# Kernel tuning notes

Measured on AMD Instinct MI355X. Metric: run time of the kernel, lower is better.

The kernel has to match this reference:

```python
import jax, jax.numpy as jnp
import numpy as np

B, T, C, H = 4, 2048, 1024, 16
HD = C // H

def setup_inputs() -> dict:
    key = jax.random.key(0)
    ks = jax.random.split(key, 9)
    s = 1.0 / np.sqrt(C)
    return {
        'x':  jax.random.normal(ks[0], (B, T, C), jnp.float32),
        'Wq': jax.random.normal(ks[1], (C, C), jnp.float32) * s,
        'bq': jnp.zeros((C,), jnp.float32),
        'Wk': jax.random.normal(ks[2], (C, C), jnp.float32) * s,
        'bk': jnp.zeros((C,), jnp.float32),
        'Wv': jax.random.normal(ks[3], (C, C), jnp.float32) * s,
        'bv': jnp.zeros((C,), jnp.float32),
        'Wo': jax.random.normal(ks[4], (C, C), jnp.float32) * s,
        'bo': jnp.zeros((C,), jnp.float32),
    }

def reference(x, Wq, bq, Wk, bk, Wv, bv, Wo, bo):
    Bx, Tx, Cx = x.shape
    # projections (torch Linear: x @ W.T + b); split heads -> (B,H,T,HD)
    def heads(y):
        return y.reshape(Bx, Tx, H, HD).transpose(0, 2, 1, 3)
    q = heads(x @ Wq.T + bq)
    k = heads(x @ Wk.T + bk)
    v = heads(x @ Wv.T + bv)
    # NOTE: original scales by 1/sqrt(embedding_dim), not head_dim
    scale = 1.0 / jnp.sqrt(jnp.asarray(Cx, x.dtype))
    att = jnp.einsum('bhqd,bhkd->bhqk', q, k) * scale
    mask = jnp.tril(jnp.ones((Tx, Tx), dtype=bool))
    att = jnp.where(mask, att, jnp.asarray(-jnp.inf, att.dtype))
    att = jax.nn.softmax(att, axis=-1)
    y = jnp.einsum('bhqk,bhkd->bhqd', att, v)
    y = y.transpose(0, 2, 1, 3).reshape(Bx, Tx, Cx)
    return y @ Wo.T + bo
```

## Files before the change

### kernel.cpp

```cpp
#include <hip/hip_runtime.h>
#include <hip/hip_bf16.h>
#include <stdint.h>

#define NB 4
#define NT 2048
#define NC 1024
#define NH 16
#define NHD 64
#define NM (NB*NT)

typedef __attribute__((ext_vector_type(8))) __bf16 bf16x8;
typedef __attribute__((ext_vector_type(4))) float floatx4;
typedef __attribute__((ext_vector_type(8))) unsigned short ushortx8;

#define AS1(p) ((const __attribute__((address_space(1))) void*)(p))
#define AS3(p) ((__attribute__((address_space(3))) void*)(p))

__device__ __forceinline__ unsigned short f2bf(float f) {
    union { float f; unsigned int u; } v; v.f = f;
    unsigned int u = v.u;
    return (unsigned short)((u + 0x7FFFu + ((u >> 16) & 1u)) >> 16);
}
__device__ __forceinline__ unsigned int pk2(float lo, float hi) {
    union { float f; unsigned int u; } a, b; a.f = hi; b.f = lo;
    return __builtin_amdgcn_perm(a.u, b.u, 0x07060302u);
}


__global__ void cast_x_tiled(const float* __restrict__ in,
                             unsigned short* __restrict__ out, int ntiles) {
    const int wid  = (blockIdx.x * blockDim.x + threadIdx.x) >> 6;
    const int lane = threadIdx.x & 63;
    if (wid >= ntiles) return;
    const int R = wid >> 5, C = wid & 31;
    const float* src = in + ((size_t)(R*16 + (lane >> 2)))*1024 + C*32 + (lane & 3)*8;
    const floatx4 v0 = *(const floatx4*)src;
    const floatx4 v1 = *(const floatx4*)(src + 4);
    ushortx8 o;
    o[0] = f2bf(v0[0]); o[1] = f2bf(v0[1]); o[2] = f2bf(v0[2]); o[3] = f2bf(v0[3]);
    o[4] = f2bf(v1[0]); o[5] = f2bf(v1[1]); o[6] = f2bf(v1[2]); o[7] = f2bf(v1[3]);
    *(ushortx8*)&out[(size_t)wid*512 + (((lane & 3)*16 + (lane >> 2)))*8] = o;
}

__global__ void cast4_tiled(const float* __restrict__ w0, const float* __restrict__ w1,
                            const float* __restrict__ w2, const float* __restrict__ w3,
                            unsigned short* __restrict__ o0, unsigned short* __restrict__ o1,
                            unsigned short* __restrict__ o2, unsigned short* __restrict__ o3,
                            int ntiles) {
    const int wid  = (blockIdx.x * blockDim.x + threadIdx.x) >> 6;
    const int lane = threadIdx.x & 63;
    if (wid >= ntiles) return;
    const float* in; unsigned short* out;
    switch (blockIdx.y) {
        case 0: in = w0; out = o0; break;
        case 1: in = w1; out = o1; break;
        case 2: in = w2; out = o2; break;
        default: in = w3; out = o3; break;
    }
    const int R = wid >> 5, C = wid & 31;
    const float* src = in + ((size_t)(R*16 + (lane >> 2)))*1024 + C*32 + (lane & 3)*8;
    const floatx4 v0 = *(const floatx4*)src;
    const floatx4 v1 = *(const floatx4*)(src + 4);
    ushortx8 o;
    o[0] = f2bf(v0[0]); o[1] = f2bf(v0[1]); o[2] = f2bf(v0[2]); o[3] = f2bf(v0[3]);
    o[4] = f2bf(v1[0]); o[5] = f2bf(v1[1]); o[6] = f2bf(v1[2]); o[7] = f2bf(v1[3]);
    *(ushortx8*)&out[(size_t)wid*512 + (((lane & 3)*16 + (lane >> 2)))*8] = o;
}

#define TM 128
#define TN 128
#define BK 32

__device__ __forceinline__ void gemm_core(
    const unsigned short* __restrict__ A,
    const unsigned short* __restrict__ W,
    const float* __restrict__ bias,
    void* __restrict__ Out,
    unsigned short* As, unsigned short* Bs,
    int m_base, int n_base, int N_out, int K, int mode, float oscale)
{
    const int tid  = threadIdx.x;
    const int lane = tid & 63;
    const int wv   = tid >> 6;
    const int quad = lane >> 4;
    const int l16  = lane & 15;
    const int wm = (wv >> 1) * 64;
    const int wn = (wv & 1) * 64;

    floatx4 acc[4][4];
    #pragma unroll
    for (int i = 0; i < 4; ++i)
        #pragma unroll
        for (int j = 0; j < 4; ++j)
            acc[i][j] = (floatx4){0.f, 0.f, 0.f, 0.f};

    const int kTiles = K / BK;
    const int kct = K >> 5;

    const unsigned short* At = A + ((size_t)((m_base >> 4) + wv*2) * kct) * 512 + (size_t)lane*8;
    const unsigned short* Wt = W + ((size_t)((n_base >> 4) + wv*2) * kct) * 512 + (size_t)lane*8;
    const size_t rstride = (size_t)kct * 512;

    for (int kt = 0; kt < kTiles; ++kt) {
        __syncthreads();
        #pragma unroll
        for (int i = 0; i < 2; ++i) {
            __builtin_amdgcn_global_load_lds(
                AS1(At + (size_t)kt*512 + i*rstride),
                AS3(&As[(wv*2 + i)*512]), 16, 0, 0);
            __builtin_amdgcn_global_load_lds(
                AS1(Wt + (size_t)kt*512 + i*rstride),
                AS3(&Bs[(wv*2 + i)*512]), 16, 0, 0);
        }
        __syncthreads();

        bf16x8 af[4], bfr[4];
        #pragma unroll
        for (int mi = 0; mi < 4; ++mi)
            af[mi] = *(const bf16x8*)&As[((wv >> 1)*4 + mi)*512 + lane*8];
        #pragma unroll
        for (int ni = 0; ni < 4; ++ni)
            bfr[ni] = *(const bf16x8*)&Bs[((wv & 1)*4 + ni)*512 + lane*8];

        #pragma unroll
        for (int mi = 0; mi < 4; ++mi)
            #pragma unroll
            for (int ni = 0; ni < 4; ++ni)
                acc[mi][ni] = __builtin_amdgcn_mfma_f32_16x16x32_bf16(
                    af[mi], bfr[ni], acc[mi][ni], 0, 0, 0);
    }

    #pragma unroll
    for (int mi = 0; mi < 4; ++mi) {
        #pragma unroll
        for (int ni = 0; ni < 4; ++ni) {
            const int col = n_base + wn + ni*16 + l16;
            const float bv = bias[col & 1023];
            #pragma unroll
            for (int r = 0; r < 4; ++r) {
                const int row = m_base + wm + mi*16 + quad*4 + r;
                const float v = (acc[mi][ni][r] + bv) * oscale;
                if (mode == 0) {
                    ((float*)Out)[(size_t)row * N_out + col] = v;
                } else if (mode == 1) {
                    const int bb = row >> 11, t = row & (NT - 1);
                    const int h  = (col >> 6) & (NH - 1), d = col & 63;
                    const int bh = bb * NH + h;
                    const size_t idx =
                        ((size_t)((bh*128 + (t >> 4))*2 + (d >> 5)))*512
                        + (size_t)((((d >> 3) & 3)*16 + (t & 15))*8 + (d & 7));
                    ((unsigned short*)Out)[idx] = f2bf(v);
                } else {
                    const int bb = row >> 11, t = row & (NT - 1);
                    const int h  = (col >> 6) & (NH - 1), hd = col & 63;
                    const int bh = bb * NH + h;
                    const int tk = t & 31;
                    const int qv = (tk >> 2) & 3;
                    const int jv = (tk & 3) + ((tk >> 4) << 2);
                    const size_t idx =
                        ((size_t)((bh*64 + (t >> 5))*4 + (hd >> 4)))*512
                        + (size_t)((qv*16 + (hd & 15))*8 + jv);
                    ((unsigned short*)Out)[idx] = f2bf(v);
                }
            }
        }
    }
}

#define QSCALE (0.03125f * 1.44269504088896340736f)

__global__ __launch_bounds__(256) void gemm_qkv(
    const unsigned short* __restrict__ A,
    const unsigned short* __restrict__ Wq, const unsigned short* __restrict__ Wk,
    const unsigned short* __restrict__ Wv,
    const float* __restrict__ bq, const float* __restrict__ bk,
    const float* __restrict__ bv,
    unsigned short* __restrict__ Qo, unsigned short* __restrict__ Ko,
    unsigned short* __restrict__ Vo)
{
    __shared__ __align__(16) unsigned short As[TM*BK];
    __shared__ __align__(16) unsigned short Bs[TN*BK];
    const int wi = blockIdx.y >> 3;
    const int n_base = (blockIdx.y & 7) * TN;
    const unsigned short* W; const float* bias; void* Out; int mode; float osc;
    if (wi == 0)      { W = Wq; bias = bq; Out = Qo; mode = 1; osc = QSCALE; }
    else if (wi == 1) { W = Wk; bias = bk; Out = Ko; mode = 1; osc = 1.0f; }
    else              { W = Wv; bias = bv; Out = Vo; mode = 2; osc = 1.0f; }
    gemm_core(A, W, bias, Out, As, Bs, blockIdx.x * TM, n_base, NC, NC, mode, osc);
}

__global__ __launch_bounds__(256) void gemm_out(
    const unsigned short* __restrict__ A,
    const unsigned short* __restrict__ W,
    const float* __restrict__ bias,
    float* __restrict__ Out)
{
    __shared__ __align__(16) unsigned short As[TM*BK];
    __shared__ __align__(16) unsigned short Bs[TN*BK];
    gemm_core(A, W, bias, Out, As, Bs, blockIdx.x * TM, blockIdx.y * TN,
              NC, NC, 0, 1.0f);
}

__device__ __forceinline__ void attn_q32(
    const unsigned short* __restrict__ Qf,
    const unsigned short* __restrict__ Kf,
    const unsigned short* __restrict__ Vf,
    unsigned short* __restrict__ Y,
    int bh, int st, int lane)
{
    const int quad = lane >> 4, l16 = lane & 15;
    const int q0 = st * 32;
    const int b = bh >> 4, h = bh & (NH - 1);

    const size_t qbase = ((size_t)(bh*128 + st*2))*1024 + (size_t)lane*8;
    const bf16x8 qa0 = *(const bf16x8*)&Qf[qbase];
    const bf16x8 qa1 = *(const bf16x8*)&Qf[qbase + 512];
    const bf16x8 qb0 = *(const bf16x8*)&Qf[qbase + 1024];
    const bf16x8 qb1 = *(const bf16x8*)&Qf[qbase + 1536];

    const unsigned short* kp = Kf + (size_t)bh*131072 + (size_t)lane*8;
    const unsigned short* vp = Vf + (size_t)bh*131072 + (size_t)lane*8;

    floatx4 oa[4], ob[4];
    #pragma unroll
    for (int nt = 0; nt < 4; ++nt) {
        oa[nt] = (floatx4){0.f,0.f,0.f,0.f};
        ob[nt] = (floatx4){0.f,0.f,0.f,0.f};
    }
    float la = 0.f, lb = 0.f;

    const int Ffull = q0 >> 6;
    const int ntile = Ffull + 1;

    for (int f = 0; f < ntile; ++f) {
        const int j0 = f * 64;
        const bool diag = (f == Ffull);
        bf16x8 kf[4][2], vf[4][2];
        {
            const unsigned short* kt = kp + (size_t)(j0 >> 4) * 1024;
            #pragma unroll
            for (int ct = 0; ct < 4; ++ct) {
                kf[ct][0] = *(const bf16x8*)&kt[ct*1024];
                kf[ct][1] = *(const bf16x8*)&kt[ct*1024 + 512];
            }
            const unsigned short* vt = vp + (size_t)(j0 >> 5) * 2048;
            #pragma unroll
            for (int nt = 0; nt < 4; ++nt) {
                vf[nt][0] = *(const bf16x8*)&vt[nt*512];
                vf[nt][1] = *(const bf16x8*)&vt[2048 + nt*512];
            }
        }
        #pragma unroll
        for (int sub = 0; sub < 2; ++sub) {
            const bf16x8 qx0 = sub ? qb0 : qa0;
            const bf16x8 qx1 = sub ? qb1 : qa1;
            floatx4* ox = sub ? ob : oa;

            floatx4 s[4];
            #pragma unroll
            for (int ct = 0; ct < 4; ++ct) {
                s[ct] = (floatx4){0.f,0.f,0.f,0.f};
                s[ct] = __builtin_amdgcn_mfma_f32_16x16x32_bf16(kf[ct][0], qx0, s[ct], 0,0,0);
                s[ct] = __builtin_amdgcn_mfma_f32_16x16x32_bf16(kf[ct][1], qx1, s[ct], 0,0,0);
            }
            float p[4][4];
            float lsum = 0.f;
            if (!diag) {
                #pragma unroll
                for (int ct = 0; ct < 4; ++ct)
                    #pragma unroll
                    for (int r = 0; r < 4; ++r) {
                        p[ct][r] = __builtin_amdgcn_exp2f(s[ct][r]);
                        lsum += p[ct][r];
                    }
            } else {
                const int row = q0 + sub*16 + l16;
                #pragma unroll
                for (int ct = 0; ct < 4; ++ct)
                    #pragma unroll
                    for (int r = 0; r < 4; ++r) {
                        const int key = j0 + ct*16 + quad*4 + r;
                        p[ct][r] = (key <= row) ? __builtin_amdgcn_exp2f(s[ct][r]) : 0.f;
                        lsum += p[ct][r];
                    }
            }
            if (sub) lb += lsum; else la += lsum;

            union { bf16x8 v; unsigned int u[4]; } pf0, pf1;
            pf0.u[0] = pk2(p[0][0], p[0][1]); pf0.u[1] = pk2(p[0][2], p[0][3]);
            pf0.u[2] = pk2(p[1][0], p[1][1]); pf0.u[3] = pk2(p[1][2], p[1][3]);
            pf1.u[0] = pk2(p[2][0], p[2][1]); pf1.u[1] = pk2(p[2][2], p[2][3]);
            pf1.u[2] = pk2(p[3][0], p[3][1]); pf1.u[3] = pk2(p[3][2], p[3][3]);

            #pragma unroll
            for (int nt = 0; nt < 4; ++nt) {
                ox[nt] = __builtin_amdgcn_mfma_f32_16x16x32_bf16(vf[nt][0], pf0.v, ox[nt], 0,0,0);
                ox[nt] = __builtin_amdgcn_mfma_f32_16x16x32_bf16(vf[nt][1], pf1.v, ox[nt], 0,0,0);
            }
        }
    }

    la += __shfl_xor(la, 16); la += __shfl_xor(la, 32);
    lb += __shfl_xor(lb, 16); lb += __shfl_xor(lb, 32);
    const float ia = 1.0f / la, ib = 1.0f / lb;

    const size_t Rbase = (size_t)((b*NT + q0) >> 4);
    const int cg = (quad >> 1), co = (quad & 1)*4;
    #pragma unroll
    for (int nt = 0; nt < 4; ++nt) {
        const size_t base = ((Rbase*32 + h*2 + (nt >> 1))*512)
                          + (size_t)((((nt & 1)*2 + cg)*16 + l16)*8 + co);
        ushort4 wa, wb;
        wa.x = f2bf(oa[nt][0]*ia); wa.y = f2bf(oa[nt][1]*ia);
        wa.z = f2bf(oa[nt][2]*ia); wa.w = f2bf(oa[nt][3]*ia);
        wb.x = f2bf(ob[nt][0]*ib); wb.y = f2bf(ob[nt][1]*ib);
        wb.z = f2bf(ob[nt][2]*ib); wb.w = f2bf(ob[nt][3]*ib);
        *(ushort4*)&Y[base]         = wa;
        *(ushort4*)&Y[base + 16384] = wb;
    }
}

__global__ __launch_bounds__(256) void flash_attn(
    const unsigned short* __restrict__ Qf,
    const unsigned short* __restrict__ Kf,
    const unsigned short* __restrict__ Vf,
    unsigned short* __restrict__ Y)
{
    const int tid  = threadIdx.x;
    const int wave = tid >> 6;
    const int lane = tid & 63;
    const int bh = blockIdx.y;
    const int w = blockIdx.x * 4 + wave;
    attn_q32(Qf, Kf, Vf, Y, bh, w, lane);
    attn_q32(Qf, Kf, Vf, Y, bh, 63 - w, lane);
}

extern "C" void kernel_launch(void* const* d_in, const int* in_sizes, int n_in,
                              void* d_out, int out_size, void* d_ws, size_t ws_size,
                              hipStream_t stream) {
    const float* x  = (const float*)d_in[0];
    const float* Wq = (const float*)d_in[1];
    const float* bq = (const float*)d_in[2];
    const float* Wk = (const float*)d_in[3];
    const float* bk = (const float*)d_in[4];
    const float* Wv = (const float*)d_in[5];
    const float* bv = (const float*)d_in[6];
    const float* Wo = (const float*)d_in[7];
    const float* bo = (const float*)d_in[8];

    char* ws = (char*)d_ws;
    size_t off = 0;
    auto alloc = [&](size_t bytes) -> void* {
        void* p = ws + off;
        off += (bytes + 255) & ~(size_t)255;
        return p;
    };
    unsigned short* xb  = (unsigned short*)alloc((size_t)NM * NC * 2);
    unsigned short* Wqb = (unsigned short*)alloc((size_t)NC * NC * 2);
    unsigned short* Wkb = (unsigned short*)alloc((size_t)NC * NC * 2);
    unsigned short* Wvb = (unsigned short*)alloc((size_t)NC * NC * 2);
    unsigned short* Wob = (unsigned short*)alloc((size_t)NC * NC * 2);
    unsigned short* Qb  = (unsigned short*)alloc((size_t)NM * NC * 2);
    unsigned short* Kb  = (unsigned short*)alloc((size_t)NM * NC * 2);
    unsigned short* Vtb = (unsigned short*)alloc((size_t)NM * NC * 2);
    unsigned short* Yb  = (unsigned short*)alloc((size_t)NM * NC * 2);

    const int ntx = NM * NC / 512;
    const int ntw = NC * NC / 512;
    cast_x_tiled<<<(ntx*64 + 255)/256, 256, 0, stream>>>(x, xb, ntx);
    cast4_tiled<<<dim3((ntw*64 + 255)/256, 4), 256, 0, stream>>>(
        Wq, Wk, Wv, Wo, Wqb, Wkb, Wvb, Wob, ntw);

    gemm_qkv<<<dim3(NM / TM, 24), 256, 0, stream>>>(
        xb, Wqb, Wkb, Wvb, bq, bk, bv, Qb, Kb, Vtb);

    flash_attn<<<dim3(8, NB*NH), 256, 0, stream>>>(Qb, Kb, Vtb, Yb);

    gemm_out<<<dim3(NM / TM, NC / TN), 256, 0, stream>>>(Yb, Wob, bo, (float*)d_out);
}
```

Measured before the change: 251.6 us.

## Replace QKV projection GEMM with 8-wave 256x256 double-buffered pipelined kernel

```diff
diff --git a/kernel.cpp b/kernel.cpp
--- a/kernel.cpp
+++ b/kernel.cpp
@@ -169,7 +169,7 @@
 
 #define QSCALE (0.03125f * 1.44269504088896340736f)
 
-__global__ __launch_bounds__(256) void gemm_qkv(
+__global__ __launch_bounds__(512, 2) void gemm_qkv8(
     const unsigned short* __restrict__ A,
     const unsigned short* __restrict__ Wq, const unsigned short* __restrict__ Wk,
     const unsigned short* __restrict__ Wv,
@@ -178,15 +178,166 @@
     unsigned short* __restrict__ Qo, unsigned short* __restrict__ Ko,
     unsigned short* __restrict__ Vo)
 {
-    __shared__ __align__(16) unsigned short As[TM*BK];
-    __shared__ __align__(16) unsigned short Bs[TN*BK];
-    const int wi = blockIdx.y >> 3;
-    const int n_base = (blockIdx.y & 7) * TN;
-    const unsigned short* W; const float* bias; void* Out; int mode; float osc;
-    if (wi == 0)      { W = Wq; bias = bq; Out = Qo; mode = 1; osc = QSCALE; }
-    else if (wi == 1) { W = Wk; bias = bk; Out = Ko; mode = 1; osc = 1.0f; }
-    else              { W = Wv; bias = bv; Out = Vo; mode = 2; osc = 1.0f; }
-    gemm_core(A, W, bias, Out, As, Bs, blockIdx.x * TM, n_base, NC, NC, mode, osc);
+    __shared__ __align__(16) unsigned short As[2][16*2*512];
+    __shared__ __align__(16) unsigned short Bs[2][16*2*512];
+
+    const int tid  = threadIdx.x;
+    const int lane = tid & 63;
+    const int wave = tid >> 6;
+    const int wm   = wave >> 2;
+    const int wn   = wave & 3;
+    const int quad = lane >> 4;
+    const int l16  = lane & 15;
+
+    const int wsel = blockIdx.y >> 2;
+    const unsigned short* W; const float* bias; unsigned short* Out;
+    int mode; float osc;
+    if (wsel == 0)      { W = Wq; bias = bq; Out = Qo; mode = 1; osc = QSCALE; }
+    else if (wsel == 1) { W = Wk; bias = bk; Out = Ko; mode = 1; osc = 1.0f; }
+    else                { W = Wv; bias = bv; Out = Vo; mode = 2; osc = 1.0f; }
+
+    const int Rb  = blockIdx.x * 16;
+    const int CTb = (blockIdx.y & 3) * 16;
+
+    const unsigned short* Ag = A + (size_t)lane * 8;
+    const unsigned short* Wg = W + (size_t)lane * 8;
+
+    const int jA  = wm*8 + wn*2;
+    const int ctB = wn*4 + wm*2;
+
+    floatx4 acc[8][4];
+    #pragma unroll
+    for (int i = 0; i < 8; ++i)
+        #pragma unroll
+        for (int j = 0; j < 4; ++j)
+            acc[i][j] = (floatx4){0.f, 0.f, 0.f, 0.f};
+
+#define SA(nbuf, j, C) __builtin_amdgcn_global_load_lds( \
+        AS1(Ag + ((size_t)(Rb + (j))*32 + (size_t)(C))*512), \
+        AS3(&As[nbuf][((j)*2 + ((C)&1))*512]), 16, 0, 0)
+#define SB(nbuf, ct, C) __builtin_amdgcn_global_load_lds( \
+        AS1(Wg + ((size_t)(CTb + (ct))*32 + (size_t)(C))*512), \
+        AS3(&Bs[nbuf][((ct)*2 + ((C)&1))*512]), 16, 0, 0)
+
+    SA(0, jA, 0); SA(0, jA+1, 0); SB(0, ctB, 0); SB(0, ctB+1, 0);
+    SA(0, jA, 1); SA(0, jA+1, 1); SB(0, ctB, 1); SB(0, ctB+1, 1);
+    asm volatile("s_waitcnt vmcnt(4)" ::: "memory");
+    __builtin_amdgcn_s_barrier();
+
+    #pragma unroll 1
+    for (int kt = 0; kt < 16; ++kt) {
+        const int cur = kt & 1, nbf = cur ^ 1;
+        const int C0 = 2*(kt+1), C1 = 2*(kt+1) + 1;
+        const bool nl = (kt < 15);
+        bf16x8 a[4], b[4];
+
+        #pragma unroll
+        for (int i = 0; i < 4; ++i)
+            a[i] = *(const bf16x8*)&As[cur][((wm*8 + i)*2 + 0)*512 + lane*8];
+        #pragma unroll
+        for (int i = 0; i < 4; ++i)
+            b[i] = *(const bf16x8*)&Bs[cur][((wn*4 + i)*2 + 0)*512 + lane*8];
+        if (nl) { SA(nbf, jA, C0); SA(nbf, jA+1, C0); }
+        __builtin_amdgcn_s_barrier();
+        __builtin_amdgcn_s_setprio(1);
+        #pragma unroll
+        for (int i = 0; i < 4; ++i)
+            #pragma unroll
+            for (int j = 0; j < 4; ++j)
+                acc[i][j] = __builtin_amdgcn_mfma_f32_16x16x32_bf16(
+                    a[i], b[j], acc[i][j], 0, 0, 0);
+        __builtin_amdgcn_s_setprio(0);
+        __builtin_amdgcn_s_barrier();
+
+        #pragma unroll
+        for (int i = 0; i < 4; ++i)
+            a[i] = *(const bf16x8*)&As[cur][((wm*8 + 4 + i)*2 + 0)*512 + lane*8];
+        if (nl) { SB(nbf, ctB, C0); SB(nbf, ctB+1, C0); }
+        __builtin_amdgcn_s_barrier();
+        __builtin_amdgcn_s_setprio(1);
+        #pragma unroll
+        for (int i = 0; i < 4; ++i)
+            #pragma unroll
+            for (int j = 0; j < 4; ++j)
+                acc[4+i][j] = __builtin_amdgcn_mfma_f32_16x16x32_bf16(
+                    a[i], b[j], acc[4+i][j], 0, 0, 0);
+        __builtin_amdgcn_s_setprio(0);
+        if (nl) asm volatile("s_waitcnt vmcnt(4)" ::: "memory");
+        else    asm volatile("s_waitcnt vmcnt(0)" ::: "memory");
+        __builtin_amdgcn_s_barrier();
+
+        #pragma unroll
+        for (int i = 0; i < 4; ++i)
+            a[i] = *(const bf16x8*)&As[cur][((wm*8 + i)*2 + 1)*512 + lane*8];
+        #pragma unroll
+        for (int i = 0; i < 4; ++i)
+            b[i] = *(const bf16x8*)&Bs[cur][((wn*4 + i)*2 + 1)*512 + lane*8];
+        if (nl) { SA(nbf, jA, C1); SA(nbf, jA+1, C1); }
+        __builtin_amdgcn_s_barrier();
+        __builtin_amdgcn_s_setprio(1);
+        #pragma unroll
+        for (int i = 0; i < 4; ++i)
+            #pragma unroll
+            for (int j = 0; j < 4; ++j)
+                acc[i][j] = __builtin_amdgcn_mfma_f32_16x16x32_bf16(
+                    a[i], b[j], acc[i][j], 0, 0, 0);
+        __builtin_amdgcn_s_setprio(0);
+        __builtin_amdgcn_s_barrier();
+
+        #pragma unroll
+        for (int i = 0; i < 4; ++i)
+            a[i] = *(const bf16x8*)&As[cur][((wm*8 + 4 + i)*2 + 1)*512 + lane*8];
+        if (nl) { SB(nbf, ctB, C1); SB(nbf, ctB+1, C1); }
+        __builtin_amdgcn_s_barrier();
+        __builtin_amdgcn_s_setprio(1);
+        #pragma unroll
+        for (int i = 0; i < 4; ++i)
+            #pragma unroll
+            for (int j = 0; j < 4; ++j)
+                acc[4+i][j] = __builtin_amdgcn_mfma_f32_16x16x32_bf16(
+                    a[i], b[j], acc[4+i][j], 0, 0, 0);
+        __builtin_amdgcn_s_setprio(0);
+        if (nl) {
+            asm volatile("s_waitcnt vmcnt(4)" ::: "memory");
+            __builtin_amdgcn_s_barrier();
+        }
+    }
+#undef SA
+#undef SB
+
+    #pragma unroll
+    for (int rf = 0; rf < 8; ++rf) {
+        #pragma unroll
+        for (int cf = 0; cf < 4; ++cf) {
+            const int col = CTb*16 + wn*64 + cf*16 + l16;
+            const float bvv = bias[col];
+            #pragma unroll
+            for (int r = 0; r < 4; ++r) {
+                const int row = Rb*16 + wm*128 + rf*16 + quad*4 + r;
+                const float v = (acc[rf][cf][r] + bvv) * osc;
+                if (mode == 1) {
+                    const int bb = row >> 11, t = row & (NT - 1);
+                    const int h  = (col >> 6) & (NH - 1), d = col & 63;
+                    const int bh = bb * NH + h;
+                    const size_t idx =
+                        ((size_t)((bh*128 + (t >> 4))*2 + (d >> 5)))*512
+                        + (size_t)((((d >> 3) & 3)*16 + (t & 15))*8 + (d & 7));
+                    Out[idx] = f2bf(v);
+                } else {
+                    const int bb = row >> 11, t = row & (NT - 1);
+                    const int h  = (col >> 6) & (NH - 1), hd = col & 63;
+                    const int bh = bb * NH + h;
+                    const int tk = t & 31;
+                    const int qv = (tk >> 2) & 3;
+                    const int jv = (tk & 3) + ((tk >> 4) << 2);
+                    const size_t idx =
+                        ((size_t)((bh*64 + (t >> 5))*4 + (hd >> 4)))*512
+                        + (size_t)((qv*16 + (hd & 15))*8 + jv);
+                    Out[idx] = f2bf(v);
+                }
+            }
+        }
+    }
 }
 
 __global__ __launch_bounds__(256) void gemm_out(
@@ -371,7 +522,7 @@
     cast4_tiled<<<dim3((ntw*64 + 255)/256, 4), 256, 0, stream>>>(
         Wq, Wk, Wv, Wo, Wqb, Wkb, Wvb, Wob, ntw);
 
-    gemm_qkv<<<dim3(NM / TM, 24), 256, 0, stream>>>(
+    gemm_qkv8<<<dim3(NM / 256, 12), 512, 0, stream>>>(
         xb, Wqb, Wkb, Wvb, bq, bk, bv, Qb, Kb, Vtb);
 
     flash_attn<<<dim3(8, NB*NH), 256, 0, stream>>>(Qb, Kb, Vtb, Yb);
```

Result: slower. 259.9 us (+3.3%).
